# Optimization experiments

Measured on AMD Instinct MI355X. Metric: run time of the kernel, lower is better.

Reference implementation:

```python
import jax, jax.numpy as jnp
import numpy as np

DIM = 512          # must equal heads*dim_head for LayerNorm(dim) on q/k to be valid
SCALE = 64 ** -0.5  # dim_head ** -0.5
EPS = 1e-5


def layer_norm(x, g, b):
    mu = jnp.mean(x, axis=-1, keepdims=True)
    var = jnp.var(x, axis=-1, keepdims=True)
    return (x - mu) * jax.lax.rsqrt(var + EPS) * g + b


def setup_inputs() -> dict:
    key = jax.random.key(0)
    ks = jax.random.split(key, 8)
    b, n, m, d = 4, 4096, 4096, DIM
    x = jax.random.normal(ks[0], (b, n, d), dtype=jnp.float32)
    context = jax.random.normal(ks[1], (b, m, d), dtype=jnp.float32)
    s = 1.0 / np.sqrt(d)
    Wq = jax.random.normal(ks[2], (d, d), dtype=jnp.float32) * s
    Wkv = jax.random.normal(ks[3], (d, 2 * d), dtype=jnp.float32) * s
    Wo = jax.random.normal(ks[4], (d, d), dtype=jnp.float32) * s
    bo = jnp.zeros((d,), dtype=jnp.float32)
    ln_g = jnp.ones((d,), dtype=jnp.float32)
    ln_b = jnp.zeros((d,), dtype=jnp.float32)
    return {"x": x, "context": context, "Wq": Wq, "Wkv": Wkv, "Wo": Wo,
            "bo": bo, "ln_g": ln_g, "ln_b": ln_b}


def reference(x, context, Wq, Wkv, Wo, bo, ln_g, ln_b):
    # linear projections (no bias on q/kv, matching nn.Linear(bias=False))
    q = x @ Wq                                   # [b, n, d]
    kv = context @ Wkv                           # [b, m, 2d]
    k, v = jnp.split(kv, 2, axis=-1)             # [b, m, d] each
    # qk-norm: same LayerNorm params applied to q and k
    q = layer_norm(q, ln_g, ln_b)
    k = layer_norm(k, ln_g, ln_b)
    # NOTE: the original never splits heads -> full-dim single-head attention
    dots = jnp.einsum('bnd,bmd->bnm', q, k) * SCALE  # [b, n, m]
    attn = jax.nn.softmax(dots, axis=-1)
    out = jnp.einsum('bnm,bmd->bnd', attn, v)        # [b, n, d]
    return out @ Wo + bo
```

## Files before the change

### kernel.cpp

```cpp
#include <hip/hip_runtime.h>

typedef __bf16 bf16_t;
typedef bf16_t bf16x8 __attribute__((ext_vector_type(8)));
typedef float f32x4 __attribute__((ext_vector_type(4)));
typedef float f32x16 __attribute__((ext_vector_type(16)));

#define DIMD 512
#define NSEQ 4096
#define BATCH 4
#define ROWS (BATCH * NSEQ)
#define MPART 2
#define FIXMAX 20.0f

__device__ __forceinline__ void gload_lds16(const bf16_t* g, bf16_t* l) {
    __builtin_amdgcn_global_load_lds((const __attribute__((address_space(1))) unsigned int*)g,
                                     (__attribute__((address_space(3))) unsigned int*)l,
                                     16, 0, 0);
}

__device__ __forceinline__ int packbf(float lo, float hi) {
    union { bf16_t h[2]; int w; } u;
    u.h[0] = (bf16_t)lo;
    u.h[1] = (bf16_t)hi;
    return u.w;
}

__global__ void detect_mode(const unsigned* __restrict__ g, int* __restrict__ mode) {
    if (threadIdx.x == 0) *mode = (*g == 0x3F800000u) ? 1 : 0;
}

__device__ __forceinline__ float cvt_in(const void* p, long i, int mode) {
    return mode ? ((const float*)p)[i] : (float)((const bf16_t*)p)[i];
}
__global__ __launch_bounds__(256) void prep(const void* __restrict__ wq,
                                            const void* __restrict__ wkv,
                                            const void* __restrict__ wo,
                                            const void* __restrict__ lng,
                                            const void* __restrict__ lnb,
                                            const void* __restrict__ bo,
                                            bf16_t* __restrict__ wqt,
                                            bf16_t* __restrict__ wkvt,
                                            bf16_t* __restrict__ wot,
                                            bf16_t* __restrict__ gq,
                                            bf16_t* __restrict__ bb,
                                            bf16_t* __restrict__ bob,
                                            const int* __restrict__ modep) {
    int mode = *modep;
    long idx = (long)blockIdx.x * 256 + threadIdx.x;
    if (idx < 262144) {
        int r = idx >> 9, c = idx & 511;
        wqt[(long)c * 512 + r] = (bf16_t)cvt_in(wq, idx, mode);
    } else if (idx < 262144 + 524288) {
        long i = idx - 262144;
        int r = i >> 10, c = i & 1023;
        wkvt[(long)c * 512 + r] = (bf16_t)cvt_in(wkv, i, mode);
    } else if (idx < 1048576) {
        long i = idx - 786432;
        int r = i >> 9, c = i & 511;
        wot[(long)c * 512 + r] = (bf16_t)cvt_in(wo, i, mode);
    } else {
        long i = idx - 1048576;
        if (i < 512) gq[i] = (bf16_t)cvt_in(lng, i, mode);
        else if (i < 1024) bb[i - 512] = (bf16_t)cvt_in(lnb, i - 512, mode);
        else if (i < 1536) bob[i - 1024] = (bf16_t)cvt_in(bo, i - 1024, mode);
    }
}

__global__ __launch_bounds__(256) void ln_rows(bf16_t* __restrict__ buf,
                                               const bf16_t* __restrict__ g,
                                               const bf16_t* __restrict__ bvec,
                                               float mult, int swz) {
    int w = threadIdx.x >> 6;
    int lane = threadIdx.x & 63;
    int row = blockIdx.x * 4 + w;
    const bf16_t* p = buf + (size_t)row * 512 + lane * 8;
    bf16x8 xv = *(const bf16x8*)p;
    float x[8];
    float s = 0.f, sq = 0.f;
#pragma unroll
    for (int i = 0; i < 8; ++i) {
        x[i] = (float)xv[i];
        s += x[i];
        sq += x[i] * x[i];
    }
#pragma unroll
    for (int off = 1; off < 64; off <<= 1) {
        s += __shfl_xor(s, off, 64);
        sq += __shfl_xor(sq, off, 64);
    }
    float mean = s * (1.0f / 512.0f);
    float var = fmaxf(sq * (1.0f / 512.0f) - mean * mean, 0.0f);
    float rstd = rsqrtf(var + 1e-5f);
    bf16x8 gv = *(const bf16x8*)(g + lane * 8);
    bf16x8 bv = *(const bf16x8*)(bvec + lane * 8);
    bf16x8 o;
#pragma unroll
    for (int i = 0; i < 8; ++i)
        o[i] = (bf16_t)(((x[i] - mean) * rstd * (float)gv[i] + (float)bv[i]) * mult);
    int outlane = swz ? (lane ^ (row & 7)) : lane;
    *(bf16x8*)(buf + (size_t)row * 512 + outlane * 8) = o;
}

template <int EPI>
__global__ __launch_bounds__(256) void gemm_nt(const void* __restrict__ A,
                                               const bf16_t* __restrict__ Bt,
                                               void* __restrict__ Cout,
                                               bf16_t* __restrict__ C2,
                                               int K, int ldc,
                                               const bf16_t* __restrict__ bias,
                                               const int* __restrict__ amodep,
                                               const int* __restrict__ omodep,
                                               const float* __restrict__ mlp) {
    __shared__ bf16_t As[64 * 32];
    __shared__ bf16_t Bs[256 * 32];
    int amode = (EPI != 2 && amodep) ? *amodep : 0;
    int t = threadIdx.x;
    int w = t >> 6;
    int lane = t & 63;
    int r16 = lane & 15;
    int quad = lane >> 4;
    int m0 = blockIdx.x * 64;
    int n0 = blockIdx.y * 256;
    int wr = w >> 1, wc = w & 1;

    f32x4 acc[2][8];
#pragma unroll
    for (int m = 0; m < 2; ++m)
#pragma unroll
        for (int n = 0; n < 8; ++n) acc[m][n] = f32x4{0.f, 0.f, 0.f, 0.f};

    int brow = w * 64 + (lane >> 2);
    int bswz = ((lane & 3) ^ ((brow >> 1) & 3)) * 8;
    const bf16_t* bsrc = Bt + (size_t)(n0 + brow) * K + bswz;
    bf16_t* bdst = Bs + (w * 64) * 32;

    int a_r = t >> 2;
    int ac = t & 3;
    bf16_t* adst = As + a_r * 32 + (ac ^ ((a_r >> 1) & 3)) * 8;

    float combine_scl = 0.f;
    if (EPI == 2)
        combine_scl = 1.0f / (mlp[m0 + a_r] + mlp[ROWS + m0 + a_r]);

    int aswz = (r16 >> 1) & 3;
    const bf16_t* abase = As + (wr * 32 + r16) * 32 + (quad ^ aswz) * 8;
    const bf16_t* bbase = Bs + (wc * 128 + r16) * 32 + (quad ^ aswz) * 8;

    for (int kt = 0; kt < K; kt += 32) {
        bf16x8 av;
        if (EPI == 2) {
            const bf16_t* r0 = (const bf16_t*)A + (size_t)(m0 + a_r) * 512 + kt + ac * 8;
            const bf16_t* r1 = r0 + (size_t)ROWS * 512;
            bf16x8 x0 = *(const bf16x8*)r0;
            bf16x8 y0 = *(const bf16x8*)r1;
#pragma unroll
            for (int j = 0; j < 8; ++j)
                av[j] = (bf16_t)(((float)x0[j] + (float)y0[j]) * combine_scl);
        } else if (amode) {
            const float* Af = (const float*)A + (size_t)(m0 + a_r) * K + kt + ac * 8;
            f32x4 lo = *(const f32x4*)Af;
            f32x4 hi = *(const f32x4*)(Af + 4);
#pragma unroll
            for (int j = 0; j < 4; ++j) { av[j] = (bf16_t)lo[j]; av[j + 4] = (bf16_t)hi[j]; }
        } else {
            av = *(const bf16x8*)((const bf16_t*)A + (size_t)(m0 + a_r) * K + kt + ac * 8);
        }
        *(bf16x8*)adst = av;
#pragma unroll
        for (int k = 0; k < 4; ++k)
            gload_lds16(bsrc + (size_t)(k * 16) * K + kt, bdst + (k * 16) * 32);
        __syncthreads();

        bf16x8 af[2], bfr[8];
#pragma unroll
        for (int m = 0; m < 2; ++m) af[m] = *(const bf16x8*)(abase + m * 16 * 32);
#pragma unroll
        for (int n = 0; n < 8; ++n) bfr[n] = *(const bf16x8*)(bbase + n * 16 * 32);
        __builtin_amdgcn_s_setprio(1);
#pragma unroll
        for (int m = 0; m < 2; ++m)
#pragma unroll
            for (int n = 0; n < 8; ++n)
                acc[m][n] = __builtin_amdgcn_mfma_f32_16x16x32_bf16(af[m], bfr[n], acc[m][n], 0, 0, 0);
        __builtin_amdgcn_s_setprio(0);
        __syncthreads();
    }

    int omode = (EPI == 2 && omodep) ? *omodep : 0;
#pragma unroll
    for (int n = 0; n < 8; ++n) {
        int col = n0 + wc * 128 + n * 16 + r16;
        float bv = (EPI == 2 && bias) ? (float)bias[col] : 0.0f;
#pragma unroll
        for (int m = 0; m < 2; ++m) {
#pragma unroll
            for (int r = 0; r < 4; ++r) {
                int row = m0 + wr * 32 + m * 16 + quad * 4 + r;
                float val = acc[m][n][r] + bv;
                if (EPI == 0) {
                    ((bf16_t*)Cout)[(size_t)row * ldc + col] = (bf16_t)val;
                } else if (EPI == 1) {
                    if (col < 512) {
                        ((bf16_t*)Cout)[(size_t)row * 512 + col] = (bf16_t)val;
                    } else {
                        int d = col - 512;
                        C2[(size_t)(row >> 5) * 16384 + (d >> 3) * 256 + ((row & 31) >> 3) * 64
                           + (d & 7) * 8 + (row & 7)] = (bf16_t)val;
                    }
                } else {
                    if (omode)
                        ((float*)Cout)[(size_t)row * 512 + col] = val;
                    else
                        ((bf16_t*)Cout)[(size_t)row * 512 + col] = (bf16_t)val;
                }
            }
        }
    }
}

__global__ __launch_bounds__(512, 2) void flash_attn(const bf16_t* __restrict__ q,
                                                     const bf16_t* __restrict__ kn,
                                                     const bf16_t* __restrict__ vt,
                                                     bf16_t* __restrict__ Opart,
                                                     float* __restrict__ ml,
                                                     const bf16_t* __restrict__ g,
                                                     const bf16_t* __restrict__ bvec) {
    __shared__ bf16_t SH[81920];
    bf16_t* Ksb0 = SH;
    bf16_t* Ksb1 = SH + 16384;
    bf16_t* Vsb0 = SH + 32768;
    bf16_t* Vsb1 = SH + 49152;
    float* Pd = (float*)(SH + 65536);

    int t = threadIdx.x;
    int w = t >> 6;
    int lane = t & 63;
    int l31 = lane & 31;
    int h = lane >> 5;
    int qb = w & 3;
    int dh = w >> 2;
    int part = blockIdx.y;
    int qrow0 = blockIdx.x * 128 + qb * 32;
    int bb = (blockIdx.x * 128) >> 12;
    int krow0 = bb * NSEQ + part * (NSEQ / MPART);
    const int niter = (NSEQ / MPART) / 32;

    {
        int r8 = lane >> 3, c8 = lane & 7;
#pragma unroll
        for (int batch = 0; batch < 2; ++batch) {
            int rloc = w * 16 + batch * 8 + r8;
            const bf16_t* src = q + (size_t)(blockIdx.x * 128 + rloc) * 512 + c8 * 64;
            bf16x8 xv[8];
            float s = 0.f, sq = 0.f;
#pragma unroll
            for (int i = 0; i < 8; ++i) {
                xv[i] = *(const bf16x8*)(src + i * 8);
#pragma unroll
                for (int j = 0; j < 8; ++j) { float f = (float)xv[i][j]; s += f; sq += f * f; }
            }
            s += __shfl_xor(s, 1, 64); sq += __shfl_xor(sq, 1, 64);
            s += __shfl_xor(s, 2, 64); sq += __shfl_xor(sq, 2, 64);
            s += __shfl_xor(s, 4, 64); sq += __shfl_xor(sq, 4, 64);
            float mean = s * (1.0f / 512.0f);
            float var = fmaxf(sq * (1.0f / 512.0f) - mean * mean, 0.0f);
            float rstd = rsqrtf(var + 1e-5f);
            bf16_t* dst = SH + rloc * 512 + c8 * 64;
#pragma unroll
            for (int i = 0; i < 8; ++i) {
                bf16x8 gv = *(const bf16x8*)(g + c8 * 64 + i * 8);
                bf16x8 bv = *(const bf16x8*)(bvec + c8 * 64 + i * 8);
                bf16x8 o;
#pragma unroll
                for (int j = 0; j < 8; ++j)
                    o[j] = (bf16_t)((((float)xv[i][j] - mean) * rstd * (float)gv[j] + (float)bv[j]) * 0.125f);
                *(bf16x8*)(dst + i * 8) = o;
            }
        }
    }
    __syncthreads();

    bf16x8 qf[16];
    {
        const bf16_t* qp = SH + (size_t)(qb * 32 + l31) * 512 + dh * 256 + h * 8;
#pragma unroll
        for (int ks = 0; ks < 16; ++ks) qf[ks] = *(const bf16x8*)(qp + ks * 16);
    }
    __syncthreads();

    f32x16 O[8];
#pragma unroll
    for (int i = 0; i < 8; ++i)
#pragma unroll
        for (int j = 0; j < 16; ++j) O[i][j] = 0.f;
    float lsum = 0.f;
    int swz7 = l31 & 7;

    const bf16_t* KbA[2] = {Ksb0 + l31 * 512, Ksb1 + l31 * 512};
    int voff = dh * 8192 + (l31 >> 3) * 256 + (l31 & 7) * 8 + h * 64;
    const bf16_t* VbA[2] = {Vsb0 + voff, Vsb1 + voff};

#define STAGE(mt, bufi)                                                                          \
    {                                                                                            \
        if (w < 4) {                                                                             \
            const bf16_t* ksrc_ = kn + (size_t)(krow0 + (mt) + w * 8) * 512 + lane * 8;          \
            bf16_t* kd_ = ((bufi) ? Ksb1 : Ksb0) + (w * 8) * 512;                                \
            _Pragma("unroll")                                                                    \
            for (int i_ = 0; i_ < 8; ++i_)                                                       \
                gload_lds16(ksrc_ + i_ * 512, kd_ + i_ * 512);                                   \
        } else {                                                                                 \
            const bf16_t* vsrc_ = vt + (size_t)((krow0 + (mt)) >> 5) * 16384                     \
                                  + (size_t)((w - 4) * 8) * 512 + lane * 8;                      \
            bf16_t* vd_ = ((bufi) ? Vsb1 : Vsb0) + ((w - 4) * 8) * 512;                          \
            _Pragma("unroll")                                                                    \
            for (int i_ = 0; i_ < 8; ++i_)                                                       \
                gload_lds16(vsrc_ + i_ * 512, vd_ + i_ * 512);                                   \
        }                                                                                        \
    }

#define FLASH_BODY(it, bufi)                                                                      \
    {                                                                                             \
        __syncthreads();                                                                          \
        if ((it) + 1 < niter) STAGE(((it) + 1) * 32, ((it) + 1) & 1);                             \
        f32x16 a;                                                                                 \
        _Pragma("unroll") for (int j = 0; j < 16; ++j) a[j] = 0.f;                                \
        __builtin_amdgcn_s_setprio(1);                                                            \
        _Pragma("unroll") for (int ks = 0; ks < 16; ++ks) {                                       \
            int fb = (dh * 32 + ks * 2 + h) ^ swz7;                                               \
            bf16x8 kf = *(const bf16x8*)(KbA[bufi] + fb * 8);                                     \
            a = __builtin_amdgcn_mfma_f32_32x32x16_bf16(kf, qf[ks], a, 0, 0, 0);                  \
        }                                                                                         \
        __builtin_amdgcn_s_setprio(0);                                                            \
        _Pragma("unroll") for (int c = 0; c < 4; ++c)                                             \
            *(f32x4*)(Pd + w * 1024 + c * 256 + lane * 4) =                                       \
                f32x4{a[4 * c], a[4 * c + 1], a[4 * c + 2], a[4 * c + 3]};                        \
        asm volatile("s_waitcnt lgkmcnt(0)" ::: "memory");    \
        __builtin_amdgcn_s_barrier();                                                             \
        asm volatile("" ::: "memory");                                                            \
        float pr[16];                                                                             \
        float ls = 0.f;                                                                           \
        _Pragma("unroll") for (int c = 0; c < 4; ++c) {                                           \
            f32x4 pp = *(const f32x4*)(Pd + (w ^ 4) * 1024 + c * 256 + lane * 4);                 \
            _Pragma("unroll") for (int j = 0; j < 4; ++j) {                                       \
                pr[4 * c + j] = __expf(a[4 * c + j] + pp[j] - FIXMAX);                            \
                ls += pr[4 * c + j];                                                              \
            }                                                                                     \
        }                                                                                         \
        lsum += ls;                                                                               \
        int pa0 = packbf(pr[0], pr[1]), pb0 = packbf(pr[4], pr[5]);                               \
        int pa1 = packbf(pr[2], pr[3]), pb1 = packbf(pr[6], pr[7]);                               \
        int pa2 = packbf(pr[8], pr[9]), pb2 = packbf(pr[12], pr[13]);                             \
        int pa3 = packbf(pr[10], pr[11]), pb3 = packbf(pr[14], pr[15]);                           \
        auto s0 = __builtin_amdgcn_permlane32_swap(pa0, pb0, false, false);                       \
        auto s1 = __builtin_amdgcn_permlane32_swap(pa1, pb1, false, false);                       \
        auto s2 = __builtin_amdgcn_permlane32_swap(pa2, pb2, false, false);                       \
        auto s3 = __builtin_amdgcn_permlane32_swap(pa3, pb3, false, false);                       \
        union { int w4[4]; bf16x8 v; } U0, U1;                                                    \
        U0.w4[0] = s0[0]; U0.w4[1] = s1[0]; U0.w4[2] = s0[1]; U0.w4[3] = s1[1];                   \
        U1.w4[0] = s2[0]; U1.w4[1] = s3[0]; U1.w4[2] = s2[1]; U1.w4[3] = s3[1];                   \
        bf16x8 pf0 = U0.v;                                     \
        bf16x8 pf1 = U1.v;                                     \
        __builtin_amdgcn_s_setprio(1);                                                            \
        _Pragma("unroll") for (int dt = 0; dt < 8; ++dt) {                                        \
            bf16x8 v0 = *(const bf16x8*)(VbA[bufi] + dt * 1024);                                  \
            bf16x8 v1 = *(const bf16x8*)(VbA[bufi] + dt * 1024 + 128);                            \
            O[dt] = __builtin_amdgcn_mfma_f32_32x32x16_bf16(pf0, v0, O[dt], 0, 0, 0);             \
            O[dt] = __builtin_amdgcn_mfma_f32_32x32x16_bf16(pf1, v1, O[dt], 0, 0, 0);             \
        }                                                                                         \
        __builtin_amdgcn_s_setprio(0);                                                            \
    }

    STAGE(0, 0);

    for (int it = 0; it < niter; it += 2) {
        FLASH_BODY(it, 0);
        FLASH_BODY(it + 1, 1);
    }

    lsum += __shfl_xor(lsum, 32, 64);
    if (dh == 0 && lane < 32) ml[(size_t)part * ROWS + qrow0 + l31] = lsum;
    bf16_t* op = Opart + (size_t)part * ROWS * 512;
#pragma unroll
    for (int dt = 0; dt < 8; ++dt)
#pragma unroll
        for (int r = 0; r < 16; ++r) {
            int qr = (r & 3) + 8 * (r >> 2) + 4 * h;
            op[(size_t)(qrow0 + qr) * 512 + dh * 256 + dt * 32 + l31] = (bf16_t)O[dt][r];
        }
#undef STAGE
#undef FLASH_BODY
}

extern "C" void kernel_launch(void* const* d_in, const int* in_sizes, int n_in,
                              void* d_out, int out_size, void* d_ws, size_t ws_size,
                              hipStream_t stream) {
    char* ws = (char*)d_ws;
    const size_t MB = 1024 * 1024;
    bf16_t* q     = (bf16_t*)(ws);
    bf16_t* kn    = (bf16_t*)(ws + 16 * MB);
    bf16_t* vt    = (bf16_t*)(ws + 32 * MB);
    bf16_t* Opart = (bf16_t*)(ws + 48 * MB);
    float*  mlbuf = (float*)(ws + 80 * MB);
    bf16_t* wqt   = (bf16_t*)(ws + 81 * MB);
    bf16_t* wkvt  = wqt + 512 * 512;
    bf16_t* wot   = wkvt + 512 * 1024;
    bf16_t* gq    = wot + 512 * 512;
    bf16_t* bb    = gq + 512;
    bf16_t* bob   = bb + 512;
    int* modep    = (int*)(bob + 512);

    detect_mode<<<1, 64, 0, stream>>>((const unsigned*)d_in[6], modep);

    prep<<<4102, 256, 0, stream>>>(d_in[2], d_in[3], d_in[4], d_in[6], d_in[7], d_in[5],
                                   wqt, wkvt, wot, gq, bb, bob, modep);

    gemm_nt<0><<<dim3(ROWS / 64, 2), 256, 0, stream>>>(d_in[0], wqt, q, nullptr, 512, 512, nullptr, modep, nullptr, nullptr);
    gemm_nt<1><<<dim3(ROWS / 64, 4), 256, 0, stream>>>(d_in[1], wkvt, kn, vt, 512, 0, nullptr, modep, nullptr, nullptr);

    ln_rows<<<dim3(ROWS / 4), 256, 0, stream>>>(kn, gq, bb, 1.0f, 1);

    flash_attn<<<dim3(ROWS / 128, MPART), 512, 0, stream>>>(q, kn, vt, Opart, mlbuf, gq, bb);

    gemm_nt<2><<<dim3(ROWS / 64, 2), 256, 0, stream>>>(Opart, wot, d_out, nullptr, 512, 512, bob, nullptr, modep, mlbuf);
}
```

Before: 386.3 us.

## Double-buffer GEMM tiles and move q LayerNorm out of flash attention

The GEMM kernel now double-buffers its A and B shared-memory tiles and prefetches the next K-tile while running MFMAs on the current one. This drops one barrier per iteration and hides global load latency, at the cost of twice the LDS. Separately, the q LayerNorm that flash_attn used to recompute in its prologue (once per M-partition) moves to a standalone ln_rows launch. This removes the duplicate normalisation and the extra shared-memory pass, but adds a kernel launch and a round trip of q through global memory. The GEMM loop now hardcodes 16 iterations, which assumes K=512.

Result: faster. 378.3 us (-2.1%).

```diff
diff --git a/kernel.cpp b/kernel.cpp
--- a/kernel.cpp
+++ b/kernel.cpp
@@ -111,8 +111,8 @@
                                                const int* __restrict__ amodep,
                                                const int* __restrict__ omodep,
                                                const float* __restrict__ mlp) {
-    __shared__ bf16_t As[64 * 32];
-    __shared__ bf16_t Bs[256 * 32];
+    __shared__ bf16_t As[2][64 * 32];
+    __shared__ bf16_t Bs[2][256 * 32];
     int amode = (EPI != 2 && amodep) ? *amodep : 0;
     int t = threadIdx.x;
     int w = t >> 6;
@@ -132,58 +132,91 @@
     int brow = w * 64 + (lane >> 2);
     int bswz = ((lane & 3) ^ ((brow >> 1) & 3)) * 8;
     const bf16_t* bsrc = Bt + (size_t)(n0 + brow) * K + bswz;
-    bf16_t* bdst = Bs + (w * 64) * 32;
+    int bdoff = (w * 64) * 32;
 
     int a_r = t >> 2;
     int ac = t & 3;
-    bf16_t* adst = As + a_r * 32 + (ac ^ ((a_r >> 1) & 3)) * 8;
+    int adoff = a_r * 32 + (ac ^ ((a_r >> 1) & 3)) * 8;
 
     float combine_scl = 0.f;
     if (EPI == 2)
         combine_scl = 1.0f / (mlp[m0 + a_r] + mlp[ROWS + m0 + a_r]);
 
     int aswz = (r16 >> 1) & 3;
-    const bf16_t* abase = As + (wr * 32 + r16) * 32 + (quad ^ aswz) * 8;
-    const bf16_t* bbase = Bs + (wc * 128 + r16) * 32 + (quad ^ aswz) * 8;
-
-    for (int kt = 0; kt < K; kt += 32) {
-        bf16x8 av;
-        if (EPI == 2) {
-            const bf16_t* r0 = (const bf16_t*)A + (size_t)(m0 + a_r) * 512 + kt + ac * 8;
-            const bf16_t* r1 = r0 + (size_t)ROWS * 512;
-            bf16x8 x0 = *(const bf16x8*)r0;
-            bf16x8 y0 = *(const bf16x8*)r1;
-#pragma unroll
-            for (int j = 0; j < 8; ++j)
-                av[j] = (bf16_t)(((float)x0[j] + (float)y0[j]) * combine_scl);
-        } else if (amode) {
-            const float* Af = (const float*)A + (size_t)(m0 + a_r) * K + kt + ac * 8;
-            f32x4 lo = *(const f32x4*)Af;
-            f32x4 hi = *(const f32x4*)(Af + 4);
-#pragma unroll
-            for (int j = 0; j < 4; ++j) { av[j] = (bf16_t)lo[j]; av[j + 4] = (bf16_t)hi[j]; }
-        } else {
-            av = *(const bf16x8*)((const bf16_t*)A + (size_t)(m0 + a_r) * K + kt + ac * 8);
-        }
-        *(bf16x8*)adst = av;
-#pragma unroll
-        for (int k = 0; k < 4; ++k)
-            gload_lds16(bsrc + (size_t)(k * 16) * K + kt, bdst + (k * 16) * 32);
-        __syncthreads();
-
-        bf16x8 af[2], bfr[8];
-#pragma unroll
-        for (int m = 0; m < 2; ++m) af[m] = *(const bf16x8*)(abase + m * 16 * 32);
-#pragma unroll
-        for (int n = 0; n < 8; ++n) bfr[n] = *(const bf16x8*)(bbase + n * 16 * 32);
-        __builtin_amdgcn_s_setprio(1);
-#pragma unroll
-        for (int m = 0; m < 2; ++m)
-#pragma unroll
-            for (int n = 0; n < 8; ++n)
-                acc[m][n] = __builtin_amdgcn_mfma_f32_16x16x32_bf16(af[m], bfr[n], acc[m][n], 0, 0, 0);
-        __builtin_amdgcn_s_setprio(0);
-        __syncthreads();
+    int aroff = (wr * 32 + r16) * 32 + (quad ^ aswz) * 8;
+    int broff = (wc * 128 + r16) * 32 + (quad ^ aswz) * 8;
+
+    bf16x8 rx, ry;
+    f32x4 rf0, rf1;
+
+#define LOAD_A(kt)                                                                               \
+    {                                                                                            \
+        if (EPI == 2) {                                                                          \
+            const bf16_t* r0_ = (const bf16_t*)A + (size_t)(m0 + a_r) * 512 + (kt) + ac * 8;     \
+            rx = *(const bf16x8*)r0_;                                                            \
+            ry = *(const bf16x8*)(r0_ + (size_t)ROWS * 512);                                     \
+        } else if (amode) {                                                                      \
+            const float* Af_ = (const float*)A + (size_t)(m0 + a_r) * K + (kt) + ac * 8;         \
+            rf0 = *(const f32x4*)Af_;                                                            \
+            rf1 = *(const f32x4*)(Af_ + 4);                                                      \
+        } else {                                                                                 \
+            rx = *(const bf16x8*)((const bf16_t*)A + (size_t)(m0 + a_r) * K + (kt) + ac * 8);    \
+        }                                                                                        \
+    }
+
+#define WRITE_A(buf)                                                                             \
+    {                                                                                            \
+        bf16x8 av_;                                                                              \
+        if (EPI == 2) {                                                                          \
+            _Pragma("unroll")                                                                    \
+            for (int j_ = 0; j_ < 8; ++j_)                                                       \
+                av_[j_] = (bf16_t)(((float)rx[j_] + (float)ry[j_]) * combine_scl);               \
+        } else if (amode) {                                                                      \
+            _Pragma("unroll")                                                                    \
+            for (int j_ = 0; j_ < 4; ++j_) { av_[j_] = (bf16_t)rf0[j_]; av_[j_ + 4] = (bf16_t)rf1[j_]; } \
+        } else {                                                                                 \
+            av_ = rx;                                                                            \
+        }                                                                                        \
+        *(bf16x8*)(&As[buf][adoff]) = av_;                                                       \
+    }
+
+#define GLOAD_B(kt, buf)                                                                         \
+    {                                                                                            \
+        _Pragma("unroll")                                                                        \
+        for (int k_ = 0; k_ < 4; ++k_)                                                           \
+            gload_lds16(bsrc + (size_t)(k_ * 16) * K + (kt), &Bs[buf][bdoff + k_ * 16 * 32]);    \
+    }
+
+#define GEMM_BODY(ki, cur)                                                                       \
+    {                                                                                            \
+        if ((ki) + 1 < 16) {                                                                     \
+            LOAD_A(((ki) + 1) * 32);                                                             \
+            GLOAD_B(((ki) + 1) * 32, (cur) ^ 1);                                                 \
+        }                                                                                        \
+        bf16x8 af[2], bfr[8];                                                                    \
+        _Pragma("unroll")                                                                        \
+        for (int m = 0; m < 2; ++m) af[m] = *(const bf16x8*)(&As[cur][aroff + m * 16 * 32]);     \
+        _Pragma("unroll")                                                                        \
+        for (int n = 0; n < 8; ++n) bfr[n] = *(const bf16x8*)(&Bs[cur][broff + n * 16 * 32]);    \
+        __builtin_amdgcn_s_setprio(1);                                                           \
+        _Pragma("unroll")                                                                        \
+        for (int m = 0; m < 2; ++m)                                                              \
+            _Pragma("unroll")                                                                    \
+            for (int n = 0; n < 8; ++n)                                                          \
+                acc[m][n] = __builtin_amdgcn_mfma_f32_16x16x32_bf16(af[m], bfr[n], acc[m][n], 0, 0, 0); \
+        __builtin_amdgcn_s_setprio(0);                                                           \
+        if ((ki) + 1 < 16) WRITE_A((cur) ^ 1);                                                   \
+        __syncthreads();                                                                         \
+    }
+
+    LOAD_A(0);
+    GLOAD_B(0, 0);
+    WRITE_A(0);
+    __syncthreads();
+
+    for (int ki = 0; ki < 16; ki += 2) {
+        GEMM_BODY(ki, 0);
+        GEMM_BODY(ki + 1, 1);
     }
 
     int omode = (EPI == 2 && omodep) ? *omodep : 0;
@@ -216,21 +249,20 @@
             }
         }
     }
+#undef LOAD_A
+#undef WRITE_A
+#undef GLOAD_B
+#undef GEMM_BODY
 }
 
 __global__ __launch_bounds__(512, 2) void flash_attn(const bf16_t* __restrict__ q,
                                                      const bf16_t* __restrict__ kn,
                                                      const bf16_t* __restrict__ vt,
                                                      bf16_t* __restrict__ Opart,
-                                                     float* __restrict__ ml,
-                                                     const bf16_t* __restrict__ g,
-                                                     const bf16_t* __restrict__ bvec) {
-    __shared__ bf16_t SH[81920];
-    bf16_t* Ksb0 = SH;
-    bf16_t* Ksb1 = SH + 16384;
-    bf16_t* Vsb0 = SH + 32768;
-    bf16_t* Vsb1 = SH + 49152;
-    float* Pd = (float*)(SH + 65536);
+                                                     float* __restrict__ ml) {
+    __shared__ bf16_t Ks[2][32 * 512];
+    __shared__ bf16_t Vs[2][32 * 512];
+    __shared__ float Pd[8][4][64][4];
 
     int t = threadIdx.x;
     int w = t >> 6;
@@ -245,48 +277,12 @@
     int krow0 = bb * NSEQ + part * (NSEQ / MPART);
     const int niter = (NSEQ / MPART) / 32;
 
-    {
-        int r8 = lane >> 3, c8 = lane & 7;
-#pragma unroll
-        for (int batch = 0; batch < 2; ++batch) {
-            int rloc = w * 16 + batch * 8 + r8;
-            const bf16_t* src = q + (size_t)(blockIdx.x * 128 + rloc) * 512 + c8 * 64;
-            bf16x8 xv[8];
-            float s = 0.f, sq = 0.f;
-#pragma unroll
-            for (int i = 0; i < 8; ++i) {
-                xv[i] = *(const bf16x8*)(src + i * 8);
-#pragma unroll
-                for (int j = 0; j < 8; ++j) { float f = (float)xv[i][j]; s += f; sq += f * f; }
-            }
-            s += __shfl_xor(s, 1, 64); sq += __shfl_xor(sq, 1, 64);
-            s += __shfl_xor(s, 2, 64); sq += __shfl_xor(sq, 2, 64);
-            s += __shfl_xor(s, 4, 64); sq += __shfl_xor(sq, 4, 64);
-            float mean = s * (1.0f / 512.0f);
-            float var = fmaxf(sq * (1.0f / 512.0f) - mean * mean, 0.0f);
-            float rstd = rsqrtf(var + 1e-5f);
-            bf16_t* dst = SH + rloc * 512 + c8 * 64;
-#pragma unroll
-            for (int i = 0; i < 8; ++i) {
-                bf16x8 gv = *(const bf16x8*)(g + c8 * 64 + i * 8);
-                bf16x8 bv = *(const bf16x8*)(bvec + c8 * 64 + i * 8);
-                bf16x8 o;
-#pragma unroll
-                for (int j = 0; j < 8; ++j)
-                    o[j] = (bf16_t)((((float)xv[i][j] - mean) * rstd * (float)gv[j] + (float)bv[j]) * 0.125f);
-                *(bf16x8*)(dst + i * 8) = o;
-            }
-        }
-    }
-    __syncthreads();
-
     bf16x8 qf[16];
     {
-        const bf16_t* qp = SH + (size_t)(qb * 32 + l31) * 512 + dh * 256 + h * 8;
+        const bf16_t* qp = q + (size_t)(qrow0 + l31) * 512 + dh * 256 + h * 8;
 #pragma unroll
         for (int ks = 0; ks < 16; ++ks) qf[ks] = *(const bf16x8*)(qp + ks * 16);
     }
-    __syncthreads();
 
     f32x16 O[8];
 #pragma unroll
@@ -296,22 +292,22 @@
     float lsum = 0.f;
     int swz7 = l31 & 7;
 
-    const bf16_t* KbA[2] = {Ksb0 + l31 * 512, Ksb1 + l31 * 512};
+    const bf16_t* KbA[2] = {&Ks[0][l31 * 512], &Ks[1][l31 * 512]};
     int voff = dh * 8192 + (l31 >> 3) * 256 + (l31 & 7) * 8 + h * 64;
-    const bf16_t* VbA[2] = {Vsb0 + voff, Vsb1 + voff};
+    const bf16_t* VbA[2] = {&Vs[0][voff], &Vs[1][voff]};
 
 #define STAGE(mt, bufi)                                                                          \
     {                                                                                            \
         if (w < 4) {                                                                             \
             const bf16_t* ksrc_ = kn + (size_t)(krow0 + (mt) + w * 8) * 512 + lane * 8;          \
-            bf16_t* kd_ = ((bufi) ? Ksb1 : Ksb0) + (w * 8) * 512;                                \
+            bf16_t* kd_ = &Ks[bufi][(w * 8) * 512];                                              \
             _Pragma("unroll")                                                                    \
             for (int i_ = 0; i_ < 8; ++i_)                                                       \
                 gload_lds16(ksrc_ + i_ * 512, kd_ + i_ * 512);                                   \
         } else {                                                                                 \
             const bf16_t* vsrc_ = vt + (size_t)((krow0 + (mt)) >> 5) * 16384                     \
                                   + (size_t)((w - 4) * 8) * 512 + lane * 8;                      \
-            bf16_t* vd_ = ((bufi) ? Vsb1 : Vsb0) + ((w - 4) * 8) * 512;                          \
+            bf16_t* vd_ = &Vs[bufi][((w - 4) * 8) * 512];                                        \
             _Pragma("unroll")                                                                    \
             for (int i_ = 0; i_ < 8; ++i_)                                                       \
                 gload_lds16(vsrc_ + i_ * 512, vd_ + i_ * 512);                                   \
@@ -332,15 +328,14 @@
         }                                                                                         \
         __builtin_amdgcn_s_setprio(0);                                                            \
         _Pragma("unroll") for (int c = 0; c < 4; ++c)                                             \
-            *(f32x4*)(Pd + w * 1024 + c * 256 + lane * 4) =                                       \
-                f32x4{a[4 * c], a[4 * c + 1], a[4 * c + 2], a[4 * c + 3]};                        \
+            *(f32x4*)&Pd[w][c][lane][0] = f32x4{a[4 * c], a[4 * c + 1], a[4 * c + 2], a[4 * c + 3]}; \
         asm volatile("s_waitcnt lgkmcnt(0)" ::: "memory");    \
         __builtin_amdgcn_s_barrier();                                                             \
         asm volatile("" ::: "memory");                                                            \
         float pr[16];                                                                             \
         float ls = 0.f;                                                                           \
         _Pragma("unroll") for (int c = 0; c < 4; ++c) {                                           \
-            f32x4 pp = *(const f32x4*)(Pd + (w ^ 4) * 1024 + c * 256 + lane * 4);                 \
+            f32x4 pp = *(const f32x4*)&Pd[w ^ 4][c][lane][0];                                     \
             _Pragma("unroll") for (int j = 0; j < 4; ++j) {                                       \
                 pr[4 * c + j] = __expf(a[4 * c + j] + pp[j] - FIXMAX);                            \
                 ls += pr[4 * c + j];                                                              \
@@ -417,9 +412,10 @@
     gemm_nt<0><<<dim3(ROWS / 64, 2), 256, 0, stream>>>(d_in[0], wqt, q, nullptr, 512, 512, nullptr, modep, nullptr, nullptr);
     gemm_nt<1><<<dim3(ROWS / 64, 4), 256, 0, stream>>>(d_in[1], wkvt, kn, vt, 512, 0, nullptr, modep, nullptr, nullptr);
 
+    ln_rows<<<dim3(ROWS / 4), 256, 0, stream>>>(q, gq, bb, 0.125f, 0);
     ln_rows<<<dim3(ROWS / 4), 256, 0, stream>>>(kn, gq, bb, 1.0f, 1);
 
-    flash_attn<<<dim3(ROWS / 128, MPART), 512, 0, stream>>>(q, kn, vt, Opart, mlbuf, gq, bb);
+    flash_attn<<<dim3(ROWS / 128, MPART), 512, 0, stream>>>(q, kn, vt, Opart, mlbuf);
 
     gemm_nt<2><<<dim3(ROWS / 64, 2), 256, 0, stream>>>(Opart, wot, d_out, nullptr, 512, 512, bob, nullptr, modep, mlbuf);
 }
```
